# Optimization experiments

Hardware: AMD Instinct MI355X
Metric: run time of the kernel (lower is better)

Reference implementation:

```python
import jax, jax.numpy as jnp
import numpy as np
from jax import lax

CHUNK = 512  # query-point chunk for pairwise point-triangle distance
EPS = 1e-12
LOSS_WEIGHT = 1.0


def closest_point_on_tri(p, a, b, c):
    """Closest point on triangle (a,b,c) to p. Broadcasts over leading dims; last dim = 3.
    Ericson, Real-Time Collision Detection, ch. 5.1.5."""
    ab = b - a
    ac = c - a
    ap = p - a
    d1 = (ab * ap).sum(-1)
    d2 = (ac * ap).sum(-1)
    bp = p - b
    d3 = (ab * bp).sum(-1)
    d4 = (ac * bp).sum(-1)
    cp_ = p - c
    d5 = (ab * cp_).sum(-1)
    d6 = (ac * cp_).sum(-1)
    va = d3 * d6 - d5 * d4
    vb = d5 * d2 - d1 * d6
    vc = d1 * d4 - d3 * d2
    # edge / interior parameters (denominators guarded; masks pick valid regions)
    v_ab = (d1 / jnp.maximum(d1 - d3, EPS))[..., None]
    w_ac = (d2 / jnp.maximum(d2 - d6, EPS))[..., None]
    w_bc = ((d4 - d3) / jnp.maximum((d4 - d3) + (d5 - d6), EPS))[..., None]
    denom = jnp.maximum(va + vb + vc, EPS)
    v_in = (vb / denom)[..., None]
    w_in = (vc / denom)[..., None]
    cond1 = ((d1 <= 0) & (d2 <= 0))[..., None]            # vertex a
    cond2 = ((d3 >= 0) & (d4 <= d3))[..., None]           # vertex b
    cond3 = ((d6 >= 0) & (d5 <= d6))[..., None]           # vertex c
    cond4 = ((vc <= 0) & (d1 >= 0) & (d3 <= 0))[..., None]  # edge ab
    cond5 = ((vb <= 0) & (d2 >= 0) & (d6 <= 0))[..., None]  # edge ac
    cond6 = ((va <= 0) & ((d4 - d3) >= 0) & ((d5 - d6) >= 0))[..., None]  # edge bc
    out = a + ab * v_in + ac * w_in                      # interior
    out = jnp.where(cond6, b + (c - b) * w_bc, out)
    out = jnp.where(cond5, a + ac * w_ac, out)
    out = jnp.where(cond4, a + ab * v_ab, out)
    out = jnp.where(cond3, c, out)
    out = jnp.where(cond2, b, out)
    out = jnp.where(cond1, a, out)
    return out


def nearest_points_on_mesh(points, verts, faces):
    """Exact nearest point on mesh surface for each query point.
    points: [P,3], verts: [V,3], faces: [F,3] int. Returns cp [P,3]."""
    ta = verts[faces[:, 0]]  # [F,3]
    tb = verts[faces[:, 1]]
    tc = verts[faces[:, 2]]

    def chunk_argmin(pc):  # pc: [CHUNK,3]
        cp = closest_point_on_tri(pc[:, None, :], ta[None], tb[None], tc[None])  # [C,F,3]
        d2 = ((pc[:, None, :] - cp) ** 2).sum(-1)  # [C,F]
        return jnp.argmin(d2, axis=1)

    P = points.shape[0]
    idx = lax.map(chunk_argmin, points.reshape(-1, CHUNK, 3)).reshape(P)
    cp = closest_point_on_tri(points, ta[idx], tb[idx], tc[idx])  # [P,3]
    return cp


def _per_batch_loss(points, verts, faces):
    cp = nearest_points_on_mesh(points, verts, faces)
    # torch.norm(resid, p=2) is the Frobenius norm of the whole [P,3] residual (scalar);
    # closest point is detached in the original autograd.Function usage.
    resid = points - lax.stop_gradient(cp)
    dist = jnp.sqrt((resid ** 2).sum())
    height = verts[:, 1].max() - verts[:, 1].min()  # bbox_3d[1]
    return dist / height


def setup_inputs() -> dict:
    key = jax.random.key(0)
    k1, k2, k3 = jax.random.split(key, 3)
    B, P, V, F = 2, 8192, 4098, 8192
    body_verts = jax.random.normal(k1, (B, P, 3), dtype=jnp.float32)
    mesh_verts = jax.random.normal(k2, (B, V, 3), dtype=jnp.float32)
    faces = jax.random.randint(k3, (B, F, 3), 0, V, dtype=jnp.int32)
    return {"body_verts": body_verts, "mesh_verts": mesh_verts, "faces": faces}


def reference(body_verts, mesh_verts, faces):
    losses = jax.vmap(_per_batch_loss)(body_verts, mesh_verts, faces)  # [B]
    return jnp.mean(losses) * LOSS_WEIGHT
```

## Files before the change

kernel.cpp:

```cpp
#include <hip/hip_runtime.h>

#define EPSF 1e-12f
constexpr int BB = 2;
constexpr int PP = 8192;
constexpr int VV = 4098;
constexpr int FF = 8192;

constexpr int SLOW_F4 = 5;
constexpr int NCONST = 24;
constexpr int PTS_PER_BLOCK = 1024;
constexpr int NSLICES = 256;
constexpr int CHUNK_T = FF / NSLICES;

typedef float f2 __attribute__((ext_vector_type(2)));

__device__ __forceinline__ f2 vfma(f2 a, f2 b, f2 c) {
#if __has_builtin(__builtin_elementwise_fma)
    return __builtin_elementwise_fma(a, b, c);
#else
    return (f2){fmaf(a.x, b.x, c.x), fmaf(a.y, b.y, c.y)};
#endif
}
__device__ __forceinline__ f2 vmin2(f2 a, f2 b) { return __builtin_elementwise_min(a, b); }
__device__ __forceinline__ f2 vmax2(f2 a, f2 b) { return __builtin_elementwise_max(a, b); }
__device__ __forceinline__ f2 bc(float s) { return (f2){s, s}; }

__device__ __forceinline__ unsigned int fkey(float f) {
    unsigned int u = __float_as_uint(f);
    return (u >> 31) ? ~u : (u | 0x80000000u);
}
__device__ __forceinline__ float funkey(unsigned int k) {
    unsigned int u = (k >> 31) ? (k ^ 0x80000000u) : ~k;
    return __uint_as_float(u);
}

__global__ __launch_bounds__(256) void precompute_kernel(
    const float* __restrict__ verts, const int* __restrict__ faces,
    float* __restrict__ pairrec, float4* __restrict__ slowrec,
    unsigned long long* __restrict__ mask, unsigned int* __restrict__ minD,
    float* __restrict__ sums, unsigned int* __restrict__ ykmin,
    unsigned int* __restrict__ ykmax)
{
    int idx = blockIdx.x * 256 + threadIdx.x;
    if (idx < BB) { sums[idx] = 0.0f; ykmin[idx] = 0xFFFFFFFFu; ykmax[idx] = 0u; }
    if (idx < BB * PP) minD[idx] = 0x7F800000u;
    if (idx >= BB * FF) return;

    int b = idx / FF;
    const float* vb = verts + (size_t)b * VV * 3;
    int i0 = faces[idx * 3 + 0];
    int i1 = faces[idx * 3 + 1];
    int i2 = faces[idx * 3 + 2];

    float ax = vb[i0*3+0], ay = vb[i0*3+1], az = vb[i0*3+2];
    float bx = vb[i1*3+0], by = vb[i1*3+1], bz = vb[i1*3+2];
    float cx = vb[i2*3+0], cy = vb[i2*3+1], cz = vb[i2*3+2];

    float abx = bx-ax, aby = by-ay, abz = bz-az;
    float acx = cx-ax, acy = cy-ay, acz = cz-az;
    float bcx = cx-bx, bcy = cy-by, bcz = cz-bz;

    {
        float4* t = slowrec + (size_t)idx * SLOW_F4;
        t[0] = make_float4(ax, ay, az, abx);
        t[1] = make_float4(bx, by, bz, aby);
        t[2] = make_float4(cx, cy, cz, abz);
        t[3] = make_float4(acx, acy, acz, bcx);
        t[4] = make_float4(bcy, bcz, 0.0f, 0.0f);
    }

    float nx = aby*acz - abz*acy;
    float ny = abz*acx - abx*acz;
    float nz = abx*acy - aby*acx;

    float ka1  = abx*ax + aby*ay + abz*az;
    float ka2  = acx*ax + acy*ay + acz*az;
    float kan  = nx*ax + ny*ay + nz*az;
    float aa   = ax*ax + ay*ay + az*az;
    float abac = abx*acx + aby*acy + abz*acz;

    float ab2 = abx*abx + aby*aby + abz*abz;
    float ac2 = acx*acx + acy*acy + acz*acz;
    float bc2 = bcx*bcx + bcy*bcy + bcz*bcz;
    float nn  = nx*nx + ny*ny + nz*nz;

    float inv_ab2 = 1.0f / fmaxf(ab2, EPSF);
    float inv_ac2 = 1.0f / fmaxf(ac2, EPSF);
    float inv_bc2 = 1.0f / fmaxf(bc2, EPSF);
    float inv_nn  = 1.0f / fmaxf(nn,  EPSF);

    bool slowtri = !((nn > 0.03f * (ab2 * ac2)) &&
                     (ab2 > 1e-4f) && (ac2 > 1e-4f) && (bc2 > 1e-4f));

    unsigned long long mb = __ballot(slowtri);
    if ((threadIdx.x & 63) == 0) mask[idx >> 6] = mb;

    float INF = __uint_as_float(0x7F800000u);
    float cvals[NCONST] = {
        abx, aby, abz, ka1,
        acx, acy, acz, ka2,
        nx,  ny,  nz,  slowtri ? INF : kan,
        ax,  ay,  az,  slowtri ? INF : aa,
        ab2, ac2, abac, bc2,
        inv_ab2, inv_ac2, inv_bc2, inv_nn
    };
    float* pr = pairrec + (size_t)(idx >> 1) * (2 * NCONST) + (idx & 1);
#pragma unroll
    for (int c = 0; c < NCONST; ++c) pr[2*c] = cvals[c];
}

__device__ __forceinline__ float tri_d2(
    float px, float py, float pz,
    float4 R0, float4 R1, float4 R2, float4 R3, float4 R4)
{
#pragma clang fp contract(off)
    float ax = R0.x, ay = R0.y, az = R0.z;
    float bx = R1.x, by = R1.y, bz = R1.z;
    float cx = R2.x, cy = R2.y, cz = R2.z;
    float abx = R0.w, aby = R1.w, abz = R2.w;
    float acx = R3.x, acy = R3.y, acz = R3.z;
    float bcx = R3.w, bcy = R4.x, bcz = R4.y;

    float apx = px - ax, apy = py - ay, apz = pz - az;
    float d1 = (abx*apx + aby*apy) + abz*apz;
    float d2 = (acx*apx + acy*apy) + acz*apz;
    float bpx = px - bx, bpy = py - by, bpz = pz - bz;
    float d3 = (abx*bpx + aby*bpy) + abz*bpz;
    float d4 = (acx*bpx + acy*bpy) + acz*bpz;
    float cqx = px - cx, cqy = py - cy, cqz = pz - cz;
    float d5 = (abx*cqx + aby*cqy) + abz*cqz;
    float d6 = (acx*cqx + acy*cqy) + acz*cqz;

    float va = d3*d6 - d5*d4;
    float vb = d5*d2 - d1*d6;
    float vc = d1*d4 - d3*d2;
    float u43 = d4 - d3;
    float u56 = d5 - d6;

    bool c1 = (d1 <= 0.0f) && (d2 <= 0.0f);
    bool c2 = (d3 >= 0.0f) && (d4 <= d3);
    bool c3 = (d6 >= 0.0f) && (d5 <= d6);
    bool c4 = (vc <= 0.0f) && (d1 >= 0.0f) && (d3 <= 0.0f);
    bool c5 = (vb <= 0.0f) && (d2 >= 0.0f) && (d6 <= 0.0f);
    bool c6 = (va <= 0.0f) && (u43 >= 0.0f) && (u56 >= 0.0f);

    int reg = c1 ? 0 : (c2 ? 1 : (c3 ? 2 : (c4 ? 3 : (c5 ? 4 : (c6 ? 5 : 6)))));

    float denom = fmaxf((va + vb) + vc, EPSF);
    float den1 = (reg == 3) ? fmaxf(d1 - d3, EPSF)
               : (reg == 5) ? fmaxf(u43 + u56, EPSF)
               : (reg == 6) ? denom : 1.0f;
    float num1 = (reg == 3) ? d1
               : (reg == 5) ? u43
               : (reg == 6) ? vb : 0.0f;
    float den2 = (reg == 4) ? fmaxf(d2 - d6, EPSF)
               : (reg == 6) ? denom : 1.0f;
    float num2 = (reg == 4) ? d2
               : (reg == 6) ? vc : 0.0f;
    float s = num1 / den1;
    float t = num2 / den2;

    bool useB = (reg == 1) || (reg == 5);
    bool useC = (reg == 2);
    float basex = useB ? bx : (useC ? cx : ax);
    float basey = useB ? by : (useC ? cy : ay);
    float basez = useB ? bz : (useC ? cz : az);
    bool e1bc = (reg == 5);
    float e1x = e1bc ? bcx : abx;
    float e1y = e1bc ? bcy : aby;
    float e1z = e1bc ? bcz : abz;

    float cpx = (basex + e1x*s) + acx*t;
    float cpy = (basey + e1y*s) + acy*t;
    float cpz = (basez + e1z*s) + acz*t;
    float rx = px - cpx, ry = py - cpy, rz = pz - cpz;
    return (rx*rx + ry*ry) + rz*rz;
}

__global__ __launch_bounds__(256) void dist_kernel(
    const float* __restrict__ pts, const f2* __restrict__ pair,
    const float4* __restrict__ sa, const unsigned long long* __restrict__ mask,
    unsigned int* __restrict__ minD)
{
    const float INF = __uint_as_float(0x7F800000u);
    int tid   = threadIdx.x;
    int pg    = blockIdx.x;
    int slice = blockIdx.y;

    int b  = pg / (PP / PTS_PER_BLOCK);
    int p0 = pg * PTS_PER_BLOCK + tid;

    float PX[4], PY[4], PZ[4];
    f2 X[4], Y[4], Z[4], W[4], m[4];
#pragma unroll
    for (int k = 0; k < 4; ++k) {
        int p = p0 + k * 256;
        PX[k] = pts[p*3+0]; PY[k] = pts[p*3+1]; PZ[k] = pts[p*3+2];
        X[k] = bc(PX[k]); Y[k] = bc(PY[k]); Z[k] = bc(PZ[k]);
        W[k] = vfma(X[k], X[k], vfma(Y[k], Y[k], Z[k] * Z[k]));
        m[k] = bc(INF);
    }

    int t0 = b * FF + slice * CHUNK_T;
    const f2* cb = pair + (size_t)(t0 >> 1) * NCONST;

    for (int tp = 0; tp < CHUNK_T / 2; ++tp) {
        const f2* c = cb + tp * NCONST;
        f2 abx=c[0], aby=c[1], abz=c[2], ka1=c[3];
        f2 acx=c[4], acy=c[5], acz=c[6], ka2=c[7];
        f2 nx=c[8],  ny=c[9],  nz=c[10], kan=c[11];
        f2 ax=c[12], ay=c[13], az=c[14], aa=c[15];
        f2 ab2=c[16], ac2=c[17], abac=c[18], bc2=c[19];
        f2 iab2=c[20], iac2=c[21], ibc2=c[22], inn=c[23];

#pragma unroll
        for (int k = 0; k < 4; ++k) {
            f2 sab = vfma(abx, X[k], vfma(aby, Y[k], abz * Z[k]));
            f2 sac = vfma(acx, X[k], vfma(acy, Y[k], acz * Z[k]));
            f2 sn  = vfma(nx,  X[k], vfma(ny,  Y[k], nz  * Z[k]));
            f2 adp = vfma(ax,  X[k], vfma(ay,  Y[k], az  * Z[k]));

            f2 d1 = sab - ka1, d2 = sac - ka2;
            f2 d3 = d1 - ab2, d4 = d2 - abac;
            f2 d5 = d1 - abac, d6 = d2 - ac2;
            f2 tpn = sn - kan;

            f2 ap2 = vfma(bc(-2.0f), adp, W[k]) + aa;
            f2 bp2 = vfma(bc(-2.0f), d1, ap2) + ab2;

            f2 sA = vmin2(vmax2(d1 * iab2, bc(0.0f)), bc(1.0f));
            f2 dAB = vfma(-sA, vfma(-sA, ab2, d1 + d1), ap2);
            f2 sC = vmin2(vmax2(d2 * iac2, bc(0.0f)), bc(1.0f));
            f2 dAC = vfma(-sC, vfma(-sC, ac2, d2 + d2), ap2);
            f2 u43 = d4 - d3;
            f2 sB = vmin2(vmax2(u43 * ibc2, bc(0.0f)), bc(1.0f));
            f2 dBC = vfma(-sB, vfma(-sB, bc2, u43 + u43), bp2);

            f2 va = vfma(d3, d6, -(d5 * d4));
            f2 vb = vfma(d5, d2, -(d1 * d6));
            f2 vc = vfma(d1, d4, -(d3 * d2));
            f2 mv = vmin2(vmin2(va, vb), vc);
            f2 dIN = (tpn * tpn) * inn;

            f2 dI;
            dI.x = (mv.x >= 0.0f) ? dIN.x : INF;
            dI.y = (mv.y >= 0.0f) ? dIN.y : INF;

            m[k] = vmin2(m[k], vmin2(vmin2(dAB, dAC), vmin2(dBC, dI)));
        }
    }

    unsigned long long bits =
        (mask[t0 >> 6] >> (t0 & 63)) & 0xFFFFFFFFull;
    while (bits) {
        int bit = __builtin_ctzll(bits);
        bits &= bits - 1;
        const float4* sb = sa + (size_t)(t0 + bit) * SLOW_F4;
        float4 S0 = sb[0], S1 = sb[1], S2 = sb[2], S3 = sb[3], S4 = sb[4];
#pragma unroll
        for (int k = 0; k < 4; ++k)
            m[k].x = fminf(m[k].x, tri_d2(PX[k], PY[k], PZ[k], S0, S1, S2, S3, S4));
    }

#pragma unroll
    for (int k = 0; k < 4; ++k) {
        float r = fminf(m[k].x, m[k].y);
        atomicMin(&minD[p0 + k*256], __float_as_uint(fmaxf(r, 0.0f)));
    }
}

__global__ __launch_bounds__(256) void reduce1_kernel(
    const unsigned int* __restrict__ minD, const float* __restrict__ verts,
    float* __restrict__ sums, unsigned int* __restrict__ ykmin,
    unsigned int* __restrict__ ykmax)
{
    int blk = blockIdx.x;
    int b = blk >> 3, part = blk & 7;
    int tid = threadIdx.x;

    float s = 0.0f;
    int i0 = part * (PP / 8), i1 = i0 + (PP / 8);
    for (int i = i0 + tid; i < i1; i += 256)
        s += __uint_as_float(minD[b * PP + i]);

    float ymin = 3.4e38f, ymax = -3.4e38f;
    int v0 = part * 513, v1 = min(v0 + 513, VV);
    for (int i = v0 + tid; i < v1; i += 256) {
        float y = verts[((size_t)b * VV + i) * 3 + 1];
        ymin = fminf(ymin, y); ymax = fmaxf(ymax, y);
    }

    for (int off = 32; off > 0; off >>= 1) {
        s += __shfl_down(s, off);
        ymin = fminf(ymin, __shfl_down(ymin, off));
        ymax = fmaxf(ymax, __shfl_down(ymax, off));
    }

    __shared__ float shs[4], shmn[4], shmx[4];
    if ((tid & 63) == 0) {
        int w = tid >> 6;
        shs[w] = s; shmn[w] = ymin; shmx[w] = ymax;
    }
    __syncthreads();
    if (tid == 0) {
        float tot = shs[0], mn = shmn[0], mx = shmx[0];
        for (int w = 1; w < 4; ++w) {
            tot += shs[w];
            mn = fminf(mn, shmn[w]);
            mx = fmaxf(mx, shmx[w]);
        }
        atomicAdd(&sums[b], tot);
        atomicMin(&ykmin[b], fkey(mn));
        atomicMax(&ykmax[b], fkey(mx));
    }
}

__global__ __launch_bounds__(64) void reduce2_kernel(
    const float* __restrict__ sums, const unsigned int* __restrict__ ykmin,
    const unsigned int* __restrict__ ykmax, float* __restrict__ out)
{
    if (threadIdx.x == 0) {
        float r = 0.0f;
        for (int b = 0; b < BB; ++b) {
            float h = funkey(ykmax[b]) - funkey(ykmin[b]);
            r += sqrtf(sums[b]) / h;
        }
        out[0] = r * 0.5f;
    }
}

extern "C" void kernel_launch(void* const* d_in, const int* in_sizes, int n_in,
                              void* d_out, int out_size, void* d_ws, size_t ws_size,
                              hipStream_t stream) {
    const float* pts   = (const float*)d_in[0];
    const float* verts = (const float*)d_in[1];
    const int*   faces = (const int*)d_in[2];
    float* out = (float*)d_out;

    char* w = (char*)d_ws;
    float* pairrec = (float*)w;
    w += (size_t)(BB * FF / 2) * (2 * NCONST) * sizeof(float);
    float4* slowrec = (float4*)w;
    w += (size_t)BB * FF * SLOW_F4 * sizeof(float4);
    unsigned long long* mask = (unsigned long long*)w;
    w += (size_t)(BB * FF / 64) * sizeof(unsigned long long);
    unsigned int* minD = (unsigned int*)w;
    w += (size_t)BB * PP * sizeof(unsigned int);
    float* sums = (float*)w;          w += BB * sizeof(float);
    unsigned int* ykmin = (unsigned int*)w; w += BB * sizeof(unsigned int);
    unsigned int* ykmax = (unsigned int*)w;

    precompute_kernel<<<(BB * FF + 255) / 256, 256, 0, stream>>>(
        verts, faces, pairrec, slowrec, mask, minD, sums, ykmin, ykmax);

    dim3 grid(BB * PP / PTS_PER_BLOCK, NSLICES);
    dist_kernel<<<grid, 256, 0, stream>>>(pts, (const f2*)pairrec, slowrec, mask, minD);

    reduce1_kernel<<<16, 256, 0, stream>>>(minD, verts, sums, ykmin, ykmax);
    reduce2_kernel<<<1, 64, 0, stream>>>(sums, ykmin, ykmax, out);
}
```

Before: 208.8 us.

## Cull triangles by plane-distance lower bound before full point-triangle evaluation

Splits each triangle pair's constants into a small plane record (normal, offset, inverse normal length) and a larger record for the rest. The plane distance squared is a lower bound on the point-triangle distance, so a wave skips a triangle pair entirely when no lane could improve its running minimum. To make the running minimum tight early, each block now covers 256 points over a 512-triangle slice instead of 1024 points over 32 triangles. This also drops the four-point-per-thread register blocking and replaces the interior select with an FMA-based penalty. In exchange it adds wave-level branch divergence, loses reuse of each loaded record across four points, and the savings depend on how effective the culling is.

```diff
diff --git a/kernel.cpp b/kernel.cpp
--- a/kernel.cpp
+++ b/kernel.cpp
@@ -7,9 +7,10 @@
 constexpr int FF = 8192;
 
 constexpr int SLOW_F4 = 5;
-constexpr int NCONST = 24;
-constexpr int PTS_PER_BLOCK = 1024;
-constexpr int NSLICES = 256;
+constexpr int SCR_ST = 12;
+constexpr int RST_ST = 40;
+constexpr int PTS_PER_BLOCK = 256;
+constexpr int NSLICES = 16;
 constexpr int CHUNK_T = FF / NSLICES;
 
 typedef float f2 __attribute__((ext_vector_type(2)));
@@ -36,8 +37,9 @@
 
 __global__ __launch_bounds__(256) void precompute_kernel(
     const float* __restrict__ verts, const int* __restrict__ faces,
-    float* __restrict__ pairrec, float4* __restrict__ slowrec,
-    unsigned long long* __restrict__ mask, unsigned int* __restrict__ minD,
+    float* __restrict__ scr, float* __restrict__ rest,
+    float4* __restrict__ slowrec, unsigned long long* __restrict__ mask,
+    unsigned int* __restrict__ minD,
     float* __restrict__ sums, unsigned int* __restrict__ ykmin,
     unsigned int* __restrict__ ykmax)
 {
@@ -96,17 +98,24 @@
     if ((threadIdx.x & 63) == 0) mask[idx >> 6] = mb;
 
     float INF = __uint_as_float(0x7F800000u);
-    float cvals[NCONST] = {
-        abx, aby, abz, ka1,
-        acx, acy, acz, ka2,
-        nx,  ny,  nz,  slowtri ? INF : kan,
-        ax,  ay,  az,  slowtri ? INF : aa,
-        ab2, ac2, abac, bc2,
-        inv_ab2, inv_ac2, inv_bc2, inv_nn
-    };
-    float* pr = pairrec + (size_t)(idx >> 1) * (2 * NCONST) + (idx & 1);
+    int half = idx & 1;
+    {
+        float* s = scr + (size_t)(idx >> 1) * SCR_ST + half;
+        s[0] = nx; s[2] = ny; s[4] = nz;
+        s[6] = slowtri ? INF : kan;
+        s[8] = inv_nn; s[10] = 0.0f;
+    }
+    {
+        float rv[19] = { abx, aby, abz, ka1,
+                         acx, acy, acz, ka2,
+                         ax,  ay,  az,  slowtri ? INF : aa,
+                         ab2, ac2, abac, bc2,
+                         inv_ab2, inv_ac2, inv_bc2 };
+        float* r = rest + (size_t)(idx >> 1) * RST_ST + half;
 #pragma unroll
-    for (int c = 0; c < NCONST; ++c) pr[2*c] = cvals[c];
+        for (int c = 0; c < 19; ++c) r[2*c] = rv[c];
+        r[38] = 0.0f;
+    }
 }
 
 __device__ __forceinline__ float tri_d2(
@@ -178,54 +187,52 @@
 }
 
 __global__ __launch_bounds__(256) void dist_kernel(
-    const float* __restrict__ pts, const f2* __restrict__ pair,
-    const float4* __restrict__ sa, const unsigned long long* __restrict__ mask,
-    unsigned int* __restrict__ minD)
+    const float* __restrict__ pts, const f2* __restrict__ scr,
+    const f2* __restrict__ rest, const float4* __restrict__ sa,
+    const unsigned long long* __restrict__ mask, unsigned int* __restrict__ minD)
 {
     const float INF = __uint_as_float(0x7F800000u);
     int tid   = threadIdx.x;
     int pg    = blockIdx.x;
     int slice = blockIdx.y;
 
-    int b  = pg / (PP / PTS_PER_BLOCK);
-    int p0 = pg * PTS_PER_BLOCK + tid;
-
-    float PX[4], PY[4], PZ[4];
-    f2 X[4], Y[4], Z[4], W[4], m[4];
-#pragma unroll
-    for (int k = 0; k < 4; ++k) {
-        int p = p0 + k * 256;
-        PX[k] = pts[p*3+0]; PY[k] = pts[p*3+1]; PZ[k] = pts[p*3+2];
-        X[k] = bc(PX[k]); Y[k] = bc(PY[k]); Z[k] = bc(PZ[k]);
-        W[k] = vfma(X[k], X[k], vfma(Y[k], Y[k], Z[k] * Z[k]));
-        m[k] = bc(INF);
-    }
+    int b = pg / (PP / PTS_PER_BLOCK);
+    int p = pg * PTS_PER_BLOCK + tid;
+
+    float PXs = pts[p*3+0], PYs = pts[p*3+1], PZs = pts[p*3+2];
+    f2 X = bc(PXs), Y = bc(PYs), Z = bc(PZs);
+    f2 W = vfma(X, X, vfma(Y, Y, Z * Z));
+    f2 m = bc(INF);
 
     int t0 = b * FF + slice * CHUNK_T;
-    const f2* cb = pair + (size_t)(t0 >> 1) * NCONST;
+    const f2* sc = scr + (size_t)(t0 >> 1) * (SCR_ST / 2);
+    const f2* rc = rest + (size_t)(t0 >> 1) * (RST_ST / 2);
 
     for (int tp = 0; tp < CHUNK_T / 2; ++tp) {
-        const f2* c = cb + tp * NCONST;
-        f2 abx=c[0], aby=c[1], abz=c[2], ka1=c[3];
-        f2 acx=c[4], acy=c[5], acz=c[6], ka2=c[7];
-        f2 nx=c[8],  ny=c[9],  nz=c[10], kan=c[11];
-        f2 ax=c[12], ay=c[13], az=c[14], aa=c[15];
-        f2 ab2=c[16], ac2=c[17], abac=c[18], bc2=c[19];
-        f2 iab2=c[20], iac2=c[21], ibc2=c[22], inn=c[23];
-
-#pragma unroll
-        for (int k = 0; k < 4; ++k) {
-            f2 sab = vfma(abx, X[k], vfma(aby, Y[k], abz * Z[k]));
-            f2 sac = vfma(acx, X[k], vfma(acy, Y[k], acz * Z[k]));
-            f2 sn  = vfma(nx,  X[k], vfma(ny,  Y[k], nz  * Z[k]));
-            f2 adp = vfma(ax,  X[k], vfma(ay,  Y[k], az  * Z[k]));
+        f2 nx = sc[0], ny = sc[1], nz = sc[2], kan = sc[3], inn = sc[4];
+        sc += SCR_ST / 2;
+
+        f2 sn  = vfma(nx, X, vfma(ny, Y, nz * Z));
+        f2 tpn = sn - kan;
+        f2 dq  = (tpn * tpn) * inn;
+        float mm = fminf(m.x, m.y);
+
+        if (__ballot((dq.x < mm) || (dq.y < mm))) {
+            f2 abx=rc[0], aby=rc[1], abz=rc[2], ka1=rc[3];
+            f2 acx=rc[4], acy=rc[5], acz=rc[6], ka2=rc[7];
+            f2 ax=rc[8],  ay=rc[9],  az=rc[10], aa=rc[11];
+            f2 ab2=rc[12], ac2=rc[13], abac=rc[14], bc2=rc[15];
+            f2 iab2=rc[16], iac2=rc[17], ibc2=rc[18];
+
+            f2 sab = vfma(abx, X, vfma(aby, Y, abz * Z));
+            f2 sac = vfma(acx, X, vfma(acy, Y, acz * Z));
+            f2 adp = vfma(ax,  X, vfma(ay,  Y, az  * Z));
 
             f2 d1 = sab - ka1, d2 = sac - ka2;
             f2 d3 = d1 - ab2, d4 = d2 - abac;
             f2 d5 = d1 - abac, d6 = d2 - ac2;
-            f2 tpn = sn - kan;
-
-            f2 ap2 = vfma(bc(-2.0f), adp, W[k]) + aa;
+
+            f2 ap2 = vfma(bc(-2.0f), adp, W) + aa;
             f2 bp2 = vfma(bc(-2.0f), d1, ap2) + ab2;
 
             f2 sA = vmin2(vmax2(d1 * iab2, bc(0.0f)), bc(1.0f));
@@ -240,33 +247,27 @@
             f2 vb = vfma(d5, d2, -(d1 * d6));
             f2 vc = vfma(d1, d4, -(d3 * d2));
             f2 mv = vmin2(vmin2(va, vb), vc);
-            f2 dIN = (tpn * tpn) * inn;
-
-            f2 dI;
-            dI.x = (mv.x >= 0.0f) ? dIN.x : INF;
-            dI.y = (mv.y >= 0.0f) ? dIN.y : INF;
-
-            m[k] = vmin2(m[k], vmin2(vmin2(dAB, dAC), vmin2(dBC, dI)));
+            f2 dI = vfma(vmin2(mv, bc(0.0f)), bc(-1e30f), dq);
+
+            m = vmin2(m, vmin2(vmin2(dAB, dAC), vmin2(dBC, dI)));
         }
-    }
-
-    unsigned long long bits =
-        (mask[t0 >> 6] >> (t0 & 63)) & 0xFFFFFFFFull;
-    while (bits) {
-        int bit = __builtin_ctzll(bits);
-        bits &= bits - 1;
-        const float4* sb = sa + (size_t)(t0 + bit) * SLOW_F4;
-        float4 S0 = sb[0], S1 = sb[1], S2 = sb[2], S3 = sb[3], S4 = sb[4];
+        rc += RST_ST / 2;
+    }
+
 #pragma unroll
-        for (int k = 0; k < 4; ++k)
-            m[k].x = fminf(m[k].x, tri_d2(PX[k], PY[k], PZ[k], S0, S1, S2, S3, S4));
-    }
-
-#pragma unroll
-    for (int k = 0; k < 4; ++k) {
-        float r = fminf(m[k].x, m[k].y);
-        atomicMin(&minD[p0 + k*256], __float_as_uint(fmaxf(r, 0.0f)));
-    }
+    for (int w = 0; w < CHUNK_T / 64; ++w) {
+        unsigned long long bits = mask[(t0 >> 6) + w];
+        while (bits) {
+            int bit = __builtin_ctzll(bits);
+            bits &= bits - 1;
+            const float4* sb = sa + (size_t)(t0 + w*64 + bit) * SLOW_F4;
+            float4 S0 = sb[0], S1 = sb[1], S2 = sb[2], S3 = sb[3], S4 = sb[4];
+            m.x = fminf(m.x, tri_d2(PXs, PYs, PZs, S0, S1, S2, S3, S4));
+        }
+    }
+
+    float r = fminf(m.x, m.y);
+    atomicMin(&minD[p], __float_as_uint(fmaxf(r, 0.0f)));
 }
 
 __global__ __launch_bounds__(256) void reduce1_kernel(
@@ -338,8 +339,10 @@
     float* out = (float*)d_out;
 
     char* w = (char*)d_ws;
-    float* pairrec = (float*)w;
-    w += (size_t)(BB * FF / 2) * (2 * NCONST) * sizeof(float);
+    float* scr = (float*)w;
+    w += (size_t)(BB * FF / 2) * SCR_ST * sizeof(float);
+    float* rest = (float*)w;
+    w += (size_t)(BB * FF / 2) * RST_ST * sizeof(float);
     float4* slowrec = (float4*)w;
     w += (size_t)BB * FF * SLOW_F4 * sizeof(float4);
     unsigned long long* mask = (unsigned long long*)w;
@@ -351,10 +354,11 @@
     unsigned int* ykmax = (unsigned int*)w;
 
     precompute_kernel<<<(BB * FF + 255) / 256, 256, 0, stream>>>(
-        verts, faces, pairrec, slowrec, mask, minD, sums, ykmin, ykmax);
+        verts, faces, scr, rest, slowrec, mask, minD, sums, ykmin, ykmax);
 
     dim3 grid(BB * PP / PTS_PER_BLOCK, NSLICES);
-    dist_kernel<<<grid, 256, 0, stream>>>(pts, (const f2*)pairrec, slowrec, mask, minD);
+    dist_kernel<<<grid, 256, 0, stream>>>(
+        pts, (const f2*)scr, (const f2*)rest, slowrec, mask, minD);
 
     reduce1_kernel<<<16, 256, 0, stream>>>(minD, verts, sums, ykmin, ykmax);
     reduce2_kernel<<<1, 64, 0, stream>>>(sums, ykmin, ykmax, out);
```

After: 265.8 us. +27.3%, slower.

## Rework interior distance algebra, double points per block, fuse final reductions

Applied to the files above, without the earlier changes.

The interior-region test now uses barycentric numerators built from d1/d2 and the triangle Gram terms, and the distance comes from ap2 minus a projected term. This drops the normal dot product and the d3..d6 intermediates, so the per-triangle record shrinks from 24 to 22 constants. Each block now processes 8 points per thread over 64-triangle slices, which halves the number of slices and gives more reuse of each constant load, at the cost of more registers (launch bounds now request 4 blocks). The two reduction kernels are folded into the distance kernel through a last-block-done counter, removing two launches but adding a serial tail in one block.

```diff
diff --git a/kernel.cpp b/kernel.cpp
--- a/kernel.cpp
+++ b/kernel.cpp
@@ -7,9 +7,9 @@
 constexpr int FF = 8192;
 
 constexpr int SLOW_F4 = 5;
-constexpr int NCONST = 24;
-constexpr int PTS_PER_BLOCK = 1024;
-constexpr int NSLICES = 256;
+constexpr int NCONST = 22;
+constexpr int PTS_PER_BLOCK = 2048;
+constexpr int NSLICES = 128;
 constexpr int CHUNK_T = FF / NSLICES;
 
 typedef float f2 __attribute__((ext_vector_type(2)));
@@ -24,25 +24,16 @@
 __device__ __forceinline__ f2 vmin2(f2 a, f2 b) { return __builtin_elementwise_min(a, b); }
 __device__ __forceinline__ f2 vmax2(f2 a, f2 b) { return __builtin_elementwise_max(a, b); }
 __device__ __forceinline__ f2 bc(float s) { return (f2){s, s}; }
-
-__device__ __forceinline__ unsigned int fkey(float f) {
-    unsigned int u = __float_as_uint(f);
-    return (u >> 31) ? ~u : (u | 0x80000000u);
-}
-__device__ __forceinline__ float funkey(unsigned int k) {
-    unsigned int u = (k >> 31) ? (k ^ 0x80000000u) : ~k;
-    return __uint_as_float(u);
-}
+__device__ __forceinline__ f2 clamp01(f2 x) { return vmin2(vmax2(x, bc(0.0f)), bc(1.0f)); }
 
 __global__ __launch_bounds__(256) void precompute_kernel(
     const float* __restrict__ verts, const int* __restrict__ faces,
     float* __restrict__ pairrec, float4* __restrict__ slowrec,
     unsigned long long* __restrict__ mask, unsigned int* __restrict__ minD,
-    float* __restrict__ sums, unsigned int* __restrict__ ykmin,
-    unsigned int* __restrict__ ykmax)
+    unsigned int* __restrict__ done)
 {
     int idx = blockIdx.x * 256 + threadIdx.x;
-    if (idx < BB) { sums[idx] = 0.0f; ykmin[idx] = 0xFFFFFFFFu; ykmax[idx] = 0u; }
+    if (idx == 0) *done = 0u;
     if (idx < BB * PP) minD[idx] = 0x7F800000u;
     if (idx >= BB * FF) return;
 
@@ -75,7 +66,6 @@
 
     float ka1  = abx*ax + aby*ay + abz*az;
     float ka2  = acx*ax + acy*ay + acz*az;
-    float kan  = nx*ax + ny*ay + nz*az;
     float aa   = ax*ax + ay*ay + az*az;
     float abac = abx*acx + aby*acy + abz*acz;
 
@@ -99,10 +89,10 @@
     float cvals[NCONST] = {
         abx, aby, abz, ka1,
         acx, acy, acz, ka2,
-        nx,  ny,  nz,  slowtri ? INF : kan,
         ax,  ay,  az,  slowtri ? INF : aa,
         ab2, ac2, abac, bc2,
-        inv_ab2, inv_ac2, inv_bc2, inv_nn
+        ab2 - abac, inv_ab2, inv_ac2, inv_bc2,
+        inv_nn, nn
     };
     float* pr = pairrec + (size_t)(idx >> 1) * (2 * NCONST) + (idx & 1);
 #pragma unroll
@@ -177,26 +167,25 @@
     return (rx*rx + ry*ry) + rz*rz;
 }
 
-__global__ __launch_bounds__(256) void dist_kernel(
+__global__ __launch_bounds__(256, 4) void dist_kernel(
     const float* __restrict__ pts, const f2* __restrict__ pair,
     const float4* __restrict__ sa, const unsigned long long* __restrict__ mask,
-    unsigned int* __restrict__ minD)
+    const float* __restrict__ verts, unsigned int* __restrict__ minD,
+    unsigned int* __restrict__ done, float* __restrict__ out)
 {
     const float INF = __uint_as_float(0x7F800000u);
     int tid   = threadIdx.x;
     int pg    = blockIdx.x;
     int slice = blockIdx.y;
 
-    int b  = pg / (PP / PTS_PER_BLOCK);
+    int b  = pg >> 2;
     int p0 = pg * PTS_PER_BLOCK + tid;
 
-    float PX[4], PY[4], PZ[4];
-    f2 X[4], Y[4], Z[4], W[4], m[4];
-#pragma unroll
-    for (int k = 0; k < 4; ++k) {
+    f2 X[8], Y[8], Z[8], W[8], m[8];
+#pragma unroll
+    for (int k = 0; k < 8; ++k) {
         int p = p0 + k * 256;
-        PX[k] = pts[p*3+0]; PY[k] = pts[p*3+1]; PZ[k] = pts[p*3+2];
-        X[k] = bc(PX[k]); Y[k] = bc(PY[k]); Z[k] = bc(PZ[k]);
+        X[k] = bc(pts[p*3+0]); Y[k] = bc(pts[p*3+1]); Z[k] = bc(pts[p*3+2]);
         W[k] = vfma(X[k], X[k], vfma(Y[k], Y[k], Z[k] * Z[k]));
         m[k] = bc(INF);
     }
@@ -208,124 +197,103 @@
         const f2* c = cb + tp * NCONST;
         f2 abx=c[0], aby=c[1], abz=c[2], ka1=c[3];
         f2 acx=c[4], acy=c[5], acz=c[6], ka2=c[7];
-        f2 nx=c[8],  ny=c[9],  nz=c[10], kan=c[11];
-        f2 ax=c[12], ay=c[13], az=c[14], aa=c[15];
-        f2 ab2=c[16], ac2=c[17], abac=c[18], bc2=c[19];
-        f2 iab2=c[20], iac2=c[21], ibc2=c[22], inn=c[23];
-
-#pragma unroll
-        for (int k = 0; k < 4; ++k) {
+        f2 ax=c[8],  ay=c[9],  az=c[10], aa=c[11];
+        f2 ab2=c[12], ac2=c[13], abac=c[14], bc2=c[15];
+        f2 kbc=c[16], iab2=c[17], iac2=c[18], ibc2=c[19];
+        f2 inn=c[20], nn=c[21];
+
+#pragma unroll
+        for (int k = 0; k < 8; ++k) {
             f2 sab = vfma(abx, X[k], vfma(aby, Y[k], abz * Z[k]));
             f2 sac = vfma(acx, X[k], vfma(acy, Y[k], acz * Z[k]));
-            f2 sn  = vfma(nx,  X[k], vfma(ny,  Y[k], nz  * Z[k]));
             f2 adp = vfma(ax,  X[k], vfma(ay,  Y[k], az  * Z[k]));
 
             f2 d1 = sab - ka1, d2 = sac - ka2;
-            f2 d3 = d1 - ab2, d4 = d2 - abac;
-            f2 d5 = d1 - abac, d6 = d2 - ac2;
-            f2 tpn = sn - kan;
-
             f2 ap2 = vfma(bc(-2.0f), adp, W[k]) + aa;
             f2 bp2 = vfma(bc(-2.0f), d1, ap2) + ab2;
 
-            f2 sA = vmin2(vmax2(d1 * iab2, bc(0.0f)), bc(1.0f));
+            f2 sA = clamp01(d1 * iab2);
             f2 dAB = vfma(-sA, vfma(-sA, ab2, d1 + d1), ap2);
-            f2 sC = vmin2(vmax2(d2 * iac2, bc(0.0f)), bc(1.0f));
+            f2 sC = clamp01(d2 * iac2);
             f2 dAC = vfma(-sC, vfma(-sC, ac2, d2 + d2), ap2);
-            f2 u43 = d4 - d3;
-            f2 sB = vmin2(vmax2(u43 * ibc2, bc(0.0f)), bc(1.0f));
+            f2 u43 = (d2 - d1) + kbc;
+            f2 sB = clamp01(u43 * ibc2);
             f2 dBC = vfma(-sB, vfma(-sB, bc2, u43 + u43), bp2);
 
-            f2 va = vfma(d3, d6, -(d5 * d4));
-            f2 vb = vfma(d5, d2, -(d1 * d6));
-            f2 vc = vfma(d1, d4, -(d3 * d2));
-            f2 mv = vmin2(vmin2(va, vb), vc);
-            f2 dIN = (tpn * tpn) * inn;
-
-            f2 dI;
-            dI.x = (mv.x >= 0.0f) ? dIN.x : INF;
-            dI.y = (mv.y >= 0.0f) ? dIN.y : INF;
+            f2 v = vfma(ac2, d1, -(abac * d2));
+            f2 w = vfma(ab2, d2, -(abac * d1));
+            f2 s = v + w;
+            f2 dprod = vfma(w, d2, v * d1);
+            f2 dIN = vfma(-dprod, inn, ap2);
+            f2 g = vmin2(vmin2(v, w), nn - s);
+            f2 dI = vfma(vmin2(g, bc(0.0f)), bc(-1e30f), dIN);
 
             m[k] = vmin2(m[k], vmin2(vmin2(dAB, dAC), vmin2(dBC, dI)));
         }
     }
 
-    unsigned long long bits =
-        (mask[t0 >> 6] >> (t0 & 63)) & 0xFFFFFFFFull;
+    unsigned long long bits = mask[t0 >> 6];
     while (bits) {
         int bit = __builtin_ctzll(bits);
         bits &= bits - 1;
         const float4* sb = sa + (size_t)(t0 + bit) * SLOW_F4;
         float4 S0 = sb[0], S1 = sb[1], S2 = sb[2], S3 = sb[3], S4 = sb[4];
 #pragma unroll
-        for (int k = 0; k < 4; ++k)
-            m[k].x = fminf(m[k].x, tri_d2(PX[k], PY[k], PZ[k], S0, S1, S2, S3, S4));
-    }
-
-#pragma unroll
-    for (int k = 0; k < 4; ++k) {
+        for (int k = 0; k < 8; ++k)
+            m[k].x = fminf(m[k].x, tri_d2(X[k].x, Y[k].x, Z[k].x, S0, S1, S2, S3, S4));
+    }
+
+#pragma unroll
+    for (int k = 0; k < 8; ++k) {
         float r = fminf(m[k].x, m[k].y);
         atomicMin(&minD[p0 + k*256], __float_as_uint(fmaxf(r, 0.0f)));
     }
-}
-
-__global__ __launch_bounds__(256) void reduce1_kernel(
-    const unsigned int* __restrict__ minD, const float* __restrict__ verts,
-    float* __restrict__ sums, unsigned int* __restrict__ ykmin,
-    unsigned int* __restrict__ ykmax)
-{
-    int blk = blockIdx.x;
-    int b = blk >> 3, part = blk & 7;
-    int tid = threadIdx.x;
-
-    float s = 0.0f;
-    int i0 = part * (PP / 8), i1 = i0 + (PP / 8);
-    for (int i = i0 + tid; i < i1; i += 256)
-        s += __uint_as_float(minD[b * PP + i]);
-
-    float ymin = 3.4e38f, ymax = -3.4e38f;
-    int v0 = part * 513, v1 = min(v0 + 513, VV);
-    for (int i = v0 + tid; i < v1; i += 256) {
-        float y = verts[((size_t)b * VV + i) * 3 + 1];
-        ymin = fminf(ymin, y); ymax = fmaxf(ymax, y);
-    }
-
+
+    __shared__ int isLast;
+    __threadfence();
+    if (tid == 0) {
+        unsigned int t = atomicAdd(done, 1u);
+        isLast = (t == (unsigned int)(gridDim.x * gridDim.y) - 1u);
+    }
+    __syncthreads();
+    if (!isLast) return;
+
+    float s0 = 0.0f, s1 = 0.0f;
+    for (int i = tid; i < PP; i += 256) {
+        s0 += __uint_as_float(atomicAdd(&minD[i], 0u));
+        s1 += __uint_as_float(atomicAdd(&minD[PP + i], 0u));
+    }
+    float mn0 = 3.4e38f, mx0 = -3.4e38f, mn1 = 3.4e38f, mx1 = -3.4e38f;
+    for (int i = tid; i < VV; i += 256) {
+        float y0 = verts[(size_t)i * 3 + 1];
+        float y1 = verts[((size_t)VV + i) * 3 + 1];
+        mn0 = fminf(mn0, y0); mx0 = fmaxf(mx0, y0);
+        mn1 = fminf(mn1, y1); mx1 = fmaxf(mx1, y1);
+    }
     for (int off = 32; off > 0; off >>= 1) {
-        s += __shfl_down(s, off);
-        ymin = fminf(ymin, __shfl_down(ymin, off));
-        ymax = fmaxf(ymax, __shfl_down(ymax, off));
-    }
-
-    __shared__ float shs[4], shmn[4], shmx[4];
+        s0 += __shfl_down(s0, off);  s1 += __shfl_down(s1, off);
+        mn0 = fminf(mn0, __shfl_down(mn0, off));
+        mx0 = fmaxf(mx0, __shfl_down(mx0, off));
+        mn1 = fminf(mn1, __shfl_down(mn1, off));
+        mx1 = fmaxf(mx1, __shfl_down(mx1, off));
+    }
+    __shared__ float sh[6][4];
     if ((tid & 63) == 0) {
         int w = tid >> 6;
-        shs[w] = s; shmn[w] = ymin; shmx[w] = ymax;
+        sh[0][w] = s0; sh[1][w] = s1;
+        sh[2][w] = mn0; sh[3][w] = mx0;
+        sh[4][w] = mn1; sh[5][w] = mx1;
     }
     __syncthreads();
     if (tid == 0) {
-        float tot = shs[0], mn = shmn[0], mx = shmx[0];
+        float t0s = sh[0][0], t1s = sh[1][0];
+        float a0 = sh[2][0], b0 = sh[3][0], a1 = sh[4][0], b1 = sh[5][0];
         for (int w = 1; w < 4; ++w) {
-            tot += shs[w];
-            mn = fminf(mn, shmn[w]);
-            mx = fmaxf(mx, shmx[w]);
+            t0s += sh[0][w]; t1s += sh[1][w];
+            a0 = fminf(a0, sh[2][w]); b0 = fmaxf(b0, sh[3][w]);
+            a1 = fminf(a1, sh[4][w]); b1 = fmaxf(b1, sh[5][w]);
         }
-        atomicAdd(&sums[b], tot);
-        atomicMin(&ykmin[b], fkey(mn));
-        atomicMax(&ykmax[b], fkey(mx));
-    }
-}
-
-__global__ __launch_bounds__(64) void reduce2_kernel(
-    const float* __restrict__ sums, const unsigned int* __restrict__ ykmin,
-    const unsigned int* __restrict__ ykmax, float* __restrict__ out)
-{
-    if (threadIdx.x == 0) {
-        float r = 0.0f;
-        for (int b = 0; b < BB; ++b) {
-            float h = funkey(ykmax[b]) - funkey(ykmin[b]);
-            r += sqrtf(sums[b]) / h;
-        }
-        out[0] = r * 0.5f;
+        out[0] = 0.5f * (sqrtf(t0s) / (b0 - a0) + sqrtf(t1s) / (b1 - a1));
     }
 }
 
@@ -346,16 +314,12 @@
     w += (size_t)(BB * FF / 64) * sizeof(unsigned long long);
     unsigned int* minD = (unsigned int*)w;
     w += (size_t)BB * PP * sizeof(unsigned int);
-    float* sums = (float*)w;          w += BB * sizeof(float);
-    unsigned int* ykmin = (unsigned int*)w; w += BB * sizeof(unsigned int);
-    unsigned int* ykmax = (unsigned int*)w;
+    unsigned int* done = (unsigned int*)w;
 
     precompute_kernel<<<(BB * FF + 255) / 256, 256, 0, stream>>>(
-        verts, faces, pairrec, slowrec, mask, minD, sums, ykmin, ykmax);
+        verts, faces, pairrec, slowrec, mask, minD, done);
 
     dim3 grid(BB * PP / PTS_PER_BLOCK, NSLICES);
-    dist_kernel<<<grid, 256, 0, stream>>>(pts, (const f2*)pairrec, slowrec, mask, minD);
-
-    reduce1_kernel<<<16, 256, 0, stream>>>(minD, verts, sums, ykmin, ykmax);
-    reduce2_kernel<<<1, 64, 0, stream>>>(sums, ykmin, ykmax, out);
-}
+    dist_kernel<<<grid, 256, 0, stream>>>(
+        pts, (const f2*)pairrec, slowrec, mask, verts, minD, done, out);
+}
```

New measurement: 220.8 us. 5.7% more time.

## Derive interior distance from barycentric terms, drop normal dot product, halve slices

Applied to the files above, without the earlier changes.

Rewrites the interior-region test and distance using the Gram-matrix form (v, w, nn - s), so the face normal no longer has to be dotted with the query point. This removes the normal and kan constants and shrinks the per-pair record from 24 to 22 floats. It also halves the slice count, so each block handles 64 triangles and the slow-triangle mask is read as a whole 64-bit word. The result is fewer FMAs per point-triangle pair and fewer atomics, at the cost of fewer blocks and possibly different rounding in the interior distance.

```diff
diff --git a/kernel.cpp b/kernel.cpp
--- a/kernel.cpp
+++ b/kernel.cpp
@@ -7,9 +7,9 @@
 constexpr int FF = 8192;
 
 constexpr int SLOW_F4 = 5;
-constexpr int NCONST = 24;
+constexpr int NCONST = 22;
 constexpr int PTS_PER_BLOCK = 1024;
-constexpr int NSLICES = 256;
+constexpr int NSLICES = 128;
 constexpr int CHUNK_T = FF / NSLICES;
 
 typedef float f2 __attribute__((ext_vector_type(2)));
@@ -24,6 +24,7 @@
 __device__ __forceinline__ f2 vmin2(f2 a, f2 b) { return __builtin_elementwise_min(a, b); }
 __device__ __forceinline__ f2 vmax2(f2 a, f2 b) { return __builtin_elementwise_max(a, b); }
 __device__ __forceinline__ f2 bc(float s) { return (f2){s, s}; }
+__device__ __forceinline__ f2 clamp01(f2 x) { return vmin2(vmax2(x, bc(0.0f)), bc(1.0f)); }
 
 __device__ __forceinline__ unsigned int fkey(float f) {
     unsigned int u = __float_as_uint(f);
@@ -75,7 +76,6 @@
 
     float ka1  = abx*ax + aby*ay + abz*az;
     float ka2  = acx*ax + acy*ay + acz*az;
-    float kan  = nx*ax + ny*ay + nz*az;
     float aa   = ax*ax + ay*ay + az*az;
     float abac = abx*acx + aby*acy + abz*acz;
 
@@ -99,10 +99,10 @@
     float cvals[NCONST] = {
         abx, aby, abz, ka1,
         acx, acy, acz, ka2,
-        nx,  ny,  nz,  slowtri ? INF : kan,
         ax,  ay,  az,  slowtri ? INF : aa,
         ab2, ac2, abac, bc2,
-        inv_ab2, inv_ac2, inv_bc2, inv_nn
+        ab2 - abac, inv_ab2, inv_ac2, inv_bc2,
+        inv_nn, nn
     };
     float* pr = pairrec + (size_t)(idx >> 1) * (2 * NCONST) + (idx & 1);
 #pragma unroll
@@ -187,16 +187,14 @@
     int pg    = blockIdx.x;
     int slice = blockIdx.y;
 
-    int b  = pg / (PP / PTS_PER_BLOCK);
+    int b  = pg >> 3;
     int p0 = pg * PTS_PER_BLOCK + tid;
 
-    float PX[4], PY[4], PZ[4];
     f2 X[4], Y[4], Z[4], W[4], m[4];
 #pragma unroll
     for (int k = 0; k < 4; ++k) {
         int p = p0 + k * 256;
-        PX[k] = pts[p*3+0]; PY[k] = pts[p*3+1]; PZ[k] = pts[p*3+2];
-        X[k] = bc(PX[k]); Y[k] = bc(PY[k]); Z[k] = bc(PZ[k]);
+        X[k] = bc(pts[p*3+0]); Y[k] = bc(pts[p*3+1]); Z[k] = bc(pts[p*3+2]);
         W[k] = vfma(X[k], X[k], vfma(Y[k], Y[k], Z[k] * Z[k]));
         m[k] = bc(INF);
     }
@@ -208,50 +206,42 @@
         const f2* c = cb + tp * NCONST;
         f2 abx=c[0], aby=c[1], abz=c[2], ka1=c[3];
         f2 acx=c[4], acy=c[5], acz=c[6], ka2=c[7];
-        f2 nx=c[8],  ny=c[9],  nz=c[10], kan=c[11];
-        f2 ax=c[12], ay=c[13], az=c[14], aa=c[15];
-        f2 ab2=c[16], ac2=c[17], abac=c[18], bc2=c[19];
-        f2 iab2=c[20], iac2=c[21], ibc2=c[22], inn=c[23];
+        f2 ax=c[8],  ay=c[9],  az=c[10], aa=c[11];
+        f2 ab2=c[12], ac2=c[13], abac=c[14], bc2=c[15];
+        f2 kbc=c[16], iab2=c[17], iac2=c[18], ibc2=c[19];
+        f2 inn=c[20], nn=c[21];
 
 #pragma unroll
         for (int k = 0; k < 4; ++k) {
             f2 sab = vfma(abx, X[k], vfma(aby, Y[k], abz * Z[k]));
             f2 sac = vfma(acx, X[k], vfma(acy, Y[k], acz * Z[k]));
-            f2 sn  = vfma(nx,  X[k], vfma(ny,  Y[k], nz  * Z[k]));
             f2 adp = vfma(ax,  X[k], vfma(ay,  Y[k], az  * Z[k]));
 
             f2 d1 = sab - ka1, d2 = sac - ka2;
-            f2 d3 = d1 - ab2, d4 = d2 - abac;
-            f2 d5 = d1 - abac, d6 = d2 - ac2;
-            f2 tpn = sn - kan;
-
             f2 ap2 = vfma(bc(-2.0f), adp, W[k]) + aa;
             f2 bp2 = vfma(bc(-2.0f), d1, ap2) + ab2;
 
-            f2 sA = vmin2(vmax2(d1 * iab2, bc(0.0f)), bc(1.0f));
+            f2 sA = clamp01(d1 * iab2);
             f2 dAB = vfma(-sA, vfma(-sA, ab2, d1 + d1), ap2);
-            f2 sC = vmin2(vmax2(d2 * iac2, bc(0.0f)), bc(1.0f));
+            f2 sC = clamp01(d2 * iac2);
             f2 dAC = vfma(-sC, vfma(-sC, ac2, d2 + d2), ap2);
-            f2 u43 = d4 - d3;
-            f2 sB = vmin2(vmax2(u43 * ibc2, bc(0.0f)), bc(1.0f));
+            f2 u43 = (d2 - d1) + kbc;
+            f2 sB = clamp01(u43 * ibc2);
             f2 dBC = vfma(-sB, vfma(-sB, bc2, u43 + u43), bp2);
 
-            f2 va = vfma(d3, d6, -(d5 * d4));
-            f2 vb = vfma(d5, d2, -(d1 * d6));
-            f2 vc = vfma(d1, d4, -(d3 * d2));
-            f2 mv = vmin2(vmin2(va, vb), vc);
-            f2 dIN = (tpn * tpn) * inn;
-
-            f2 dI;
-            dI.x = (mv.x >= 0.0f) ? dIN.x : INF;
-            dI.y = (mv.y >= 0.0f) ? dIN.y : INF;
+            f2 v = vfma(ac2, d1, -(abac * d2));
+            f2 w = vfma(ab2, d2, -(abac * d1));
+            f2 s = v + w;
+            f2 dprod = vfma(w, d2, v * d1);
+            f2 dIN = vfma(-dprod, inn, ap2);
+            f2 g = vmin2(vmin2(v, w), nn - s);
+            f2 dI = vfma(vmin2(g, bc(0.0f)), bc(-1e30f), dIN);
 
             m[k] = vmin2(m[k], vmin2(vmin2(dAB, dAC), vmin2(dBC, dI)));
         }
     }
 
-    unsigned long long bits =
-        (mask[t0 >> 6] >> (t0 & 63)) & 0xFFFFFFFFull;
+    unsigned long long bits = mask[t0 >> 6];
     while (bits) {
         int bit = __builtin_ctzll(bits);
         bits &= bits - 1;
@@ -259,7 +249,7 @@
         float4 S0 = sb[0], S1 = sb[1], S2 = sb[2], S3 = sb[3], S4 = sb[4];
 #pragma unroll
         for (int k = 0; k < 4; ++k)
-            m[k].x = fminf(m[k].x, tri_d2(PX[k], PY[k], PZ[k], S0, S1, S2, S3, S4));
+            m[k].x = fminf(m[k].x, tri_d2(X[k].x, Y[k].x, Z[k].x, S0, S1, S2, S3, S4));
     }
 
 #pragma unroll
@@ -354,7 +344,8 @@
         verts, faces, pairrec, slowrec, mask, minD, sums, ykmin, ykmax);
 
     dim3 grid(BB * PP / PTS_PER_BLOCK, NSLICES);
-    dist_kernel<<<grid, 256, 0, stream>>>(pts, (const f2*)pairrec, slowrec, mask, minD);
+    dist_kernel<<<grid, 256, 0, stream>>>(
+        pts, (const f2*)pairrec, slowrec, mask, minD);
 
     reduce1_kernel<<<16, 256, 0, stream>>>(minD, verts, sums, ykmin, ykmax);
     reduce2_kernel<<<1, 64, 0, stream>>>(sums, ykmin, ykmax, out);
```

Result: faster. 199.4 us (-4.5%).
